# Performance work log

Hardware: AMD Instinct MI355X
Metric: run time of the kernel (lower is better)

The kernel has to match this reference:

```python
import jax, jax.numpy as jnp
import numpy as np

B, F, T, D = 50000, 256, 1000, 6      # batch, features, trees, tree depth
N = 2 ** (D + 1) - 1                   # 127 nodes per perfect tree (heap layout)
# nodes 0 .. 2**D-2 are internal; nodes 2**D-1 .. N-1 are leaves.
# split_cond holds split thresholds at internal nodes and leaf gains at leaves
# (mirrors XGBoost JSON where leaf values live in split_conditions).

def setup_inputs() -> dict:
    key = jax.random.key(0)
    k1, k2, k3 = jax.random.split(key, 3)
    x = jax.random.normal(k1, (B, F), dtype=jnp.float32)
    split_idx = jax.random.randint(k2, (T, N), 0, F).astype(jnp.int32)  # leaf slots unused
    split_cond = jax.random.normal(k3, (T, N), dtype=jnp.float32)
    base_score = jnp.float32(0.5)
    return {"x": x, "split_idx": split_idx, "split_cond": split_cond, "base_score": base_score}

def reference(x, split_idx, split_cond, base_score):
    # Eval-mode forward: heaviside(x[:, idx] - cond, 0) hard routing, summed over trees.
    t_idx = jnp.arange(T)[None, :]                 # (1, T) tree index for advanced indexing
    node = jnp.zeros((x.shape[0], T), jnp.int32)   # (B, T) current node per sample/tree
    for _ in range(D):
        feat = split_idx[t_idx, node]              # (B, T)
        cond = split_cond[t_idx, node]             # (B, T)
        xv = jnp.take_along_axis(x, feat, axis=1)  # (B, T) gather features
        # torch.heaviside(c, 0): weight = 1 iff c > 0 -> go right; ties go left.
        w = (xv - cond > 0).astype(jnp.int32)
        node = 2 * node + 1 + w                    # heap child
    leaf = split_cond[t_idx, node]                 # (B, T) leaf gains
    return leaf.sum(axis=-1) + base_score          # (B,)
```

## Files before the change

kernel.cpp:

```cpp
#include <hip/hip_runtime.h>
#include <stdint.h>


#define NFEAT   256
#define NNODES  127
#define NTREES  1000
#define TPAD    1024
#define SPB     64
#define NTH     512
#define TILE_T  64
#define MID_DW  128
#define NTILES  16
#define FULLB   768
#define LEFT    14
#define SLICES  16

#define MID_OFF  0
#define LEAF_OFF (TPAD * 512)
#define WS_NEED  (TPAD * 512 + TPAD * 256)

typedef __attribute__((address_space(1))) const unsigned char ga_u8;
typedef __attribute__((address_space(3))) unsigned char       la_u8;

__global__ void xgb_init_kernel(const float* __restrict__ base_score,
                                float* __restrict__ out, int B)
{
    const int i = blockIdx.x * 256 + threadIdx.x;
    if (i < B) out[i] = base_score[0];
}

__global__ void xgb_pack_kernel(const int* __restrict__ idx,
                                const float* __restrict__ cond,
                                char* __restrict__ ws)
{
    const int i = blockIdx.x * 256 + threadIdx.x;
    if (i >= TPAD * NNODES) return;
    const int t  = i / NNODES;
    const int nd = i - t * NNODES;
    int   f = 0;
    float c = 0.0f;
    if (t < NTREES) { f = idx[i]; c = cond[i]; }
    if (nd < 63) {
        int* mid = (int*)(ws + MID_OFF) + (size_t)t * MID_DW;
        mid[2 * nd]     = f;
        mid[2 * nd + 1] = __float_as_int(c);
    } else {
        ((float*)(ws + LEAF_OFF))[t * 64 + (nd - 63)] = c;
    }
}

__device__ __forceinline__ void stage_mid(const char* __restrict__ midG,
                                          int tileIdx, char* dst,
                                          int wid, int lane)
{
    const char* src = midG + (size_t)tileIdx * (TILE_T * 512);
    for (int c = wid; c < 32; c += 8) {
        const char* g = src + c * 1024 + lane * 16;
        char*       l = dst + c * 1024;
#if __has_builtin(__builtin_amdgcn_global_load_lds)
        __builtin_amdgcn_global_load_lds((ga_u8*)(uintptr_t)g,
                                         (la_u8*)(uintptr_t)l, 16, 0, 0);
#else
        *reinterpret_cast<int4*>(l + lane * 16) =
            *reinterpret_cast<const int4*>(g);
#endif
    }
}

__global__ __launch_bounds__(NTH, 1) void xgb_forest_kernel(
    const float* __restrict__ x,
    const char*  __restrict__ ws,
    const float* __restrict__ base_score,
    float* __restrict__ out, int B)
{
    __shared__ float xT[NFEAT * SPB];
    __shared__ __align__(16) int midL[2][TILE_T * MID_DW];
    __shared__ float partials[8 * SPB];

    const char*  midG  = ws + MID_OFF;
    const float* leafG = (const float*)(ws + LEAF_OFF);

    const int tid = threadIdx.x;
    const int bid = blockIdx.x;
    const int s   = tid & 63;
    const int wid = tid >> 6;

    int sTile, tTile0, nTiles;
    if (bid < FULLB) {
        sTile = bid;            tTile0 = 0;        nTiles = NTILES;
    } else {
        const int u = bid - FULLB;
        sTile = FULLB + (u >> 4); tTile0 = u & 15; nTiles = 1;
    }
    const int sbase = sTile * SPB;

    stage_mid(midG, tTile0, (char*)midL[0], wid, s);
    if (nTiles > 1) stage_mid(midG, tTile0 + 1, (char*)midL[1], wid, s);

    {
        const int sq = tid & 15;
        const int cg = tid >> 4;
        for (int rg = 0; rg < 4; ++rg) {
            const int  sl = rg * 16 + sq;
            const bool ok = (sbase + sl) < B;
            for (int ci = 0; ci < 2; ++ci) {
                const int c4 = ci * 32 + cg;
                float4 v = make_float4(0.f, 0.f, 0.f, 0.f);
                if (ok)
                    v = *reinterpret_cast<const float4*>(
                        &x[(size_t)(sbase + sl) * NFEAT + c4 * 4]);
                xT[(c4 * 4 + 0) * SPB + sl] = v.x;
                xT[(c4 * 4 + 1) * SPB + sl] = v.y;
                xT[(c4 * 4 + 2) * SPB + sl] = v.z;
                xT[(c4 * 4 + 3) * SPB + sl] = v.w;
            }
        }
    }
    __syncthreads();

    const float* xs = &xT[s];
    float acc = 0.0f;

    for (int t = 0; t < nTiles; ++t) {
        const int* mbuf = midL[t & 1];
        const int  tgB  = (tTile0 + t) * TILE_T + wid * 8;
        const int  lb   = wid * 8 * MID_DW;

        int node[8];
#pragma unroll
        for (int j = 0; j < 8; ++j) node[j] = 0;

#pragma unroll
        for (int d = 0; d < 6; ++d) {
#pragma unroll
            for (int j = 0; j < 8; ++j) {
                const int2 nd = *reinterpret_cast<const int2*>(
                    &mbuf[lb + j * MID_DW + 2 * node[j]]);
                const float xv = xs[nd.x * SPB];
                node[j] = 2 * node[j] + 1 +
                          (int)((xv - __int_as_float(nd.y)) > 0.0f);
            }
        }

#pragma unroll
        for (int j = 0; j < 8; ++j)
            acc += leafG[(size_t)(tgB + j) * 64 + (node[j] - 63)];

        __syncthreads();
        if (t + 2 < nTiles)
            stage_mid(midG, tTile0 + t + 2, (char*)midL[t & 1], wid, s);
    }

    partials[wid * SPB + s] = acc;
    __syncthreads();
    if (tid < SPB && sbase + tid < B) {
        float r = 0.0f;
#pragma unroll
        for (int l = 0; l < 8; ++l) r += partials[l * SPB + tid];
        if (bid < FULLB) out[sbase + tid] = r + base_score[0];
        else             atomicAdd(&out[sbase + tid], r);
    }
}

__global__ void xgb_naive_kernel(const float* __restrict__ x,
                                 const int*   __restrict__ split_idx,
                                 const float* __restrict__ split_cond,
                                 const float* __restrict__ base_score,
                                 float* __restrict__ out, int B)
{
    const int sI = blockIdx.x * 256 + threadIdx.x;
    if (sI >= B) return;
    float acc = base_score[0];
    for (int t = 0; t < NTREES; ++t) {
        int node = 0;
        for (int d = 0; d < 6; ++d) {
            const int g = t * NNODES + node;
            const float xv = x[(size_t)sI * NFEAT + split_idx[g]];
            node = 2 * node + 1 + (int)((xv - split_cond[g]) > 0.0f);
        }
        acc += split_cond[t * NNODES + node];
    }
    out[sI] = acc;
}

extern "C" void kernel_launch(void* const* d_in, const int* in_sizes, int n_in,
                              void* d_out, int out_size, void* d_ws, size_t ws_size,
                              hipStream_t stream)
{
    const float* x          = (const float*)d_in[0];
    const int*   split_idx  = (const int*)d_in[1];
    const float* split_cond = (const float*)d_in[2];
    const float* base_score = (const float*)d_in[3];
    float*       out        = (float*)d_out;

    const int B = out_size;

    if (ws_size < (size_t)WS_NEED) {
        xgb_naive_kernel<<<(B + 255) / 256, 256, 0, stream>>>(
            x, split_idx, split_cond, base_score, out, B);
        return;
    }

    xgb_init_kernel<<<(B + 255) / 256, 256, 0, stream>>>(base_score, out, B);

    xgb_pack_kernel<<<(TPAD * NNODES + 255) / 256, 256, 0, stream>>>(
        split_idx, split_cond, (char*)d_ws);

    const int grid = FULLB + LEFT * SLICES;
    xgb_forest_kernel<<<grid, NTH, 0, stream>>>(
        x, (const char*)d_ws, base_score, out, B);
}
```

Measured before the change: 134.3 us.

## Give each wave private tree staging buffers and drop block barrier; fold init into pack

Each wave now stages only its own 8 trees' internal-node data into a per-wave double buffer, so the per-tile __syncthreads is replaced by a wave-local s_waitcnt on outstanding loads. The separate init kernel is removed and the base_score initialization of the tail outputs is folded into the pack kernel, saving one launch. The risk is the hand-written vmcnt wait: it also counts the leaf global loads, so its correctness relies on the ordering of in-flight loads, and the first buffer's readiness before the first tile relies on the existing barrier after the x transpose.

Result: faster. 116.7 us (median of 2 runs) (-13.1%).

```diff
diff --git a/kernel.cpp b/kernel.cpp
--- a/kernel.cpp
+++ b/kernel.cpp
@@ -9,6 +9,7 @@
 #define SPB     64
 #define NTH     512
 #define TILE_T  64
+#define TPW     8
 #define MID_DW  128
 #define NTILES  16
 #define FULLB   768
@@ -22,18 +23,14 @@
 typedef __attribute__((address_space(1))) const unsigned char ga_u8;
 typedef __attribute__((address_space(3))) unsigned char       la_u8;
 
-__global__ void xgb_init_kernel(const float* __restrict__ base_score,
-                                float* __restrict__ out, int B)
-{
-    const int i = blockIdx.x * 256 + threadIdx.x;
-    if (i < B) out[i] = base_score[0];
-}
-
 __global__ void xgb_pack_kernel(const int* __restrict__ idx,
                                 const float* __restrict__ cond,
-                                char* __restrict__ ws)
+                                char* __restrict__ ws,
+                                const float* __restrict__ base_score,
+                                float* __restrict__ out, int B)
 {
     const int i = blockIdx.x * 256 + threadIdx.x;
+    if (i < B - FULLB * SPB) out[FULLB * SPB + i] = base_score[0];
     if (i >= TPAD * NNODES) return;
     const int t  = i / NNODES;
     const int nd = i - t * NNODES;
@@ -49,20 +46,20 @@
     }
 }
 
-__device__ __forceinline__ void stage_mid(const char* __restrict__ midG,
-                                          int tileIdx, char* dst,
-                                          int wid, int lane)
-{
-    const char* src = midG + (size_t)tileIdx * (TILE_T * 512);
-    for (int c = wid; c < 32; c += 8) {
-        const char* g = src + c * 1024 + lane * 16;
-        char*       l = dst + c * 1024;
+__device__ __forceinline__ void stage_wave(const char* __restrict__ midG,
+                                           int tileIdx, char* dst,
+                                           int wid, int lane)
+{
+    const char* src = midG + ((size_t)tileIdx * TILE_T + wid * TPW) * 512;
+#pragma unroll
+    for (int c = 0; c < 4; ++c) {
 #if __has_builtin(__builtin_amdgcn_global_load_lds)
-        __builtin_amdgcn_global_load_lds((ga_u8*)(uintptr_t)g,
-                                         (la_u8*)(uintptr_t)l, 16, 0, 0);
+        __builtin_amdgcn_global_load_lds(
+            (ga_u8*)(uintptr_t)(src + c * 1024 + lane * 16),
+            (la_u8*)(uintptr_t)(dst + c * 1024), 16, 0, 0);
 #else
-        *reinterpret_cast<int4*>(l + lane * 16) =
-            *reinterpret_cast<const int4*>(g);
+        *reinterpret_cast<int4*>(dst + c * 1024 + lane * 16) =
+            *reinterpret_cast<const int4*>(src + c * 1024 + lane * 16);
 #endif
     }
 }
@@ -74,7 +71,7 @@
     float* __restrict__ out, int B)
 {
     __shared__ float xT[NFEAT * SPB];
-    __shared__ __align__(16) int midL[2][TILE_T * MID_DW];
+    __shared__ __align__(16) int midL[8][2][TPW * MID_DW];
     __shared__ float partials[8 * SPB];
 
     const char*  midG  = ws + MID_OFF;
@@ -87,15 +84,15 @@
 
     int sTile, tTile0, nTiles;
     if (bid < FULLB) {
-        sTile = bid;            tTile0 = 0;        nTiles = NTILES;
+        sTile = bid;              tTile0 = 0;        nTiles = NTILES;
     } else {
         const int u = bid - FULLB;
-        sTile = FULLB + (u >> 4); tTile0 = u & 15; nTiles = 1;
+        sTile = FULLB + (u >> 4); tTile0 = u & 15;   nTiles = 1;
     }
     const int sbase = sTile * SPB;
 
-    stage_mid(midG, tTile0, (char*)midL[0], wid, s);
-    if (nTiles > 1) stage_mid(midG, tTile0 + 1, (char*)midL[1], wid, s);
+    stage_wave(midG, tTile0, (char*)midL[wid][0], wid, s);
+    if (nTiles > 1) stage_wave(midG, tTile0 + 1, (char*)midL[wid][1], wid, s);
 
     {
         const int sq = tid & 15;
@@ -122,20 +119,19 @@
     float acc = 0.0f;
 
     for (int t = 0; t < nTiles; ++t) {
-        const int* mbuf = midL[t & 1];
-        const int  tgB  = (tTile0 + t) * TILE_T + wid * 8;
-        const int  lb   = wid * 8 * MID_DW;
-
-        int node[8];
-#pragma unroll
-        for (int j = 0; j < 8; ++j) node[j] = 0;
+        const int* mbuf = &midL[wid][t & 1][0];
+        const int  tgB  = (tTile0 + t) * TILE_T + wid * TPW;
+
+        int node[TPW];
+#pragma unroll
+        for (int j = 0; j < TPW; ++j) node[j] = 0;
 
 #pragma unroll
         for (int d = 0; d < 6; ++d) {
 #pragma unroll
-            for (int j = 0; j < 8; ++j) {
+            for (int j = 0; j < TPW; ++j) {
                 const int2 nd = *reinterpret_cast<const int2*>(
-                    &mbuf[lb + j * MID_DW + 2 * node[j]]);
+                    &mbuf[j * MID_DW + 2 * node[j]]);
                 const float xv = xs[nd.x * SPB];
                 node[j] = 2 * node[j] + 1 +
                           (int)((xv - __int_as_float(nd.y)) > 0.0f);
@@ -143,12 +139,13 @@
         }
 
 #pragma unroll
-        for (int j = 0; j < 8; ++j)
+        for (int j = 0; j < TPW; ++j)
             acc += leafG[(size_t)(tgB + j) * 64 + (node[j] - 63)];
 
-        __syncthreads();
         if (t + 2 < nTiles)
-            stage_mid(midG, tTile0 + t + 2, (char*)midL[t & 1], wid, s);
+            stage_wave(midG, tTile0 + t + 2, (char*)midL[wid][t & 1], wid, s);
+
+        asm volatile("s_waitcnt vmcnt(4)" ::: "memory");
     }
 
     partials[wid * SPB + s] = acc;
@@ -201,10 +198,8 @@
         return;
     }
 
-    xgb_init_kernel<<<(B + 255) / 256, 256, 0, stream>>>(base_score, out, B);
-
     xgb_pack_kernel<<<(TPAD * NNODES + 255) / 256, 256, 0, stream>>>(
-        split_idx, split_cond, (char*)d_ws);
+        split_idx, split_cond, (char*)d_ws, base_score, out, B);
 
     const int grid = FULLB + LEFT * SLICES;
     xgb_forest_kernel<<<grid, NTH, 0, stream>>>(
```
